# Kernel tuning notes

Measured on AMD Instinct MI355X. Metric: run time of the kernel, lower is better.

The kernel has to match this reference:

```python
import jax, jax.numpy as jnp
import numpy as np

N_EMBD = 1024
N_HEAD = 16
HEAD_DIM = N_EMBD // N_HEAD


def setup_inputs() -> dict:
    key = jax.random.key(0)
    ks = jax.random.split(key, 5)
    B, T, C = 2, 2048, N_EMBD
    scale = 0.02
    return {
        "x": jax.random.normal(ks[0], (B, T, C), dtype=jnp.float32),
        "w_attn": jax.random.normal(ks[1], (C, 3 * C), dtype=jnp.float32) * scale,
        "b_attn": jax.random.normal(ks[2], (3 * C,), dtype=jnp.float32) * scale,
        "w_proj": jax.random.normal(ks[3], (C, C), dtype=jnp.float32) * scale,
        "b_proj": jax.random.normal(ks[4], (C,), dtype=jnp.float32) * scale,
    }


def reference(x, w_attn, b_attn, w_proj, b_proj):
    B, T, C = x.shape
    H, D = N_HEAD, HEAD_DIM
    qkv = x @ w_attn + b_attn  # [B,T,3C]
    q, k, v = jnp.split(qkv, 3, axis=-1)
    # [B,T,C] -> [B,H,T,D]
    q = q.reshape(B, T, H, D).transpose(0, 2, 1, 3)
    k = k.reshape(B, T, H, D).transpose(0, 2, 1, 3)
    v = v.reshape(B, T, H, D).transpose(0, 2, 1, 3)
    scores = jnp.einsum("bhqd,bhkd->bhqk", q, k) / jnp.sqrt(jnp.float32(D))
    causal = jnp.tril(jnp.ones((T, T), dtype=bool))
    scores = jnp.where(causal, scores, jnp.finfo(scores.dtype).min)
    attn = jax.nn.softmax(scores, axis=-1)
    y = jnp.einsum("bhqk,bhkd->bhqd", attn, v)  # [B,H,T,D]
    y = y.transpose(0, 2, 1, 3).reshape(B, T, C)
    return y @ w_proj + b_proj
```

## Files before the change

kernel.cpp:

```cpp
#include <hip/hip_runtime.h>

typedef unsigned short u16;
typedef u16 u16x4 __attribute__((ext_vector_type(4)));
typedef u16 u16x8 __attribute__((ext_vector_type(8)));
typedef __bf16 bf16x8 __attribute__((ext_vector_type(8)));
typedef float floatx4 __attribute__((ext_vector_type(4)));

#define N_EMBD 1024
#define N_HEAD 16
#define HEAD_DIM 64
#define SEQ 2048
#define BATCH 2
#define M_ROWS (BATCH * SEQ)

typedef __attribute__((address_space(1))) const unsigned char ga_t;
typedef __attribute__((address_space(3))) unsigned char la_t;

#if __has_builtin(__builtin_amdgcn_exp2f)
#define EXP2(x) __builtin_amdgcn_exp2f(x)
#else
#define EXP2(x) exp2f(x)
#endif

__device__ __forceinline__ u16 cvt_bf16(float f) {
  return __builtin_bit_cast(u16, (__bf16)f);
}

__global__ __launch_bounds__(256) void prep(const float* __restrict__ x,
                                            u16* __restrict__ xb,
                                            const float* __restrict__ wa,
                                            const float* __restrict__ wp,
                                            u16* __restrict__ outa,
                                            u16* __restrict__ outp) {
  const int bid = blockIdx.x;
  if (bid < 2048) {
    const long i = ((long)bid * 256 + threadIdx.x) * 8;
    const float4 f0 = *(const float4*)&x[i];
    const float4 f1 = *(const float4*)&x[i + 4];
    u16x8 p;
    p[0] = cvt_bf16(f0.x); p[1] = cvt_bf16(f0.y);
    p[2] = cvt_bf16(f0.z); p[3] = cvt_bf16(f0.w);
    p[4] = cvt_bf16(f1.x); p[5] = cvt_bf16(f1.y);
    p[6] = cvt_bf16(f1.z); p[7] = cvt_bf16(f1.w);
    *(u16x8*)&xb[i] = p;
    return;
  }
  __shared__ u16 tile[32][33];
  const int t = bid - 2048;
  const int gx = t & 127;
  const int gy = t >> 7;
  const int R = N_EMBD;
  const float* in;
  u16* out;
  int C, bx;
  if (gx < 96) {
    in = wa; out = outa; C = 3 * N_EMBD; bx = gx * 32;
  } else {
    in = wp; out = outp; C = N_EMBD; bx = (gx - 96) * 32;
  }
  const int by = gy * 32;
  const int tx = threadIdx.x & 31;
  const int ty = threadIdx.x >> 5;
#pragma unroll
  for (int j = 0; j < 32; j += 8)
    tile[ty + j][tx] = cvt_bf16(in[(long)(by + ty + j) * C + bx + tx]);
  __syncthreads();
#pragma unroll
  for (int j = 0; j < 32; j += 8)
    out[(long)(bx + ty + j) * R + by + tx] = tile[tx][ty + j];
}

#define BK 32

template <int MODE>
__global__ __launch_bounds__(256) void gemm128(
    const u16* __restrict__ A, const u16* __restrict__ Bt,
    const float* __restrict__ bias, float* __restrict__ out,
    u16* __restrict__ qo, u16* __restrict__ ko, u16* __restrict__ vo, int N,
    int K) {
  __shared__ u16 As[128 * BK];
  __shared__ u16 Bs[128 * BK];
  const int tid = threadIdx.x;
  const int bm = blockIdx.y * 128;
  const int bn = blockIdx.x * 128;
  const int w = tid >> 6;
  const int l = tid & 63;
  const int wm = (w >> 1) * 64;
  const int wn = (w & 1) * 64;
  const int m16 = l & 15;
  const int quad = l >> 4;
  const int lrow = l >> 2;
  const int lcol = (l & 3) * 8;

  floatx4 acc[4][4];
#pragma unroll
  for (int i = 0; i < 4; ++i)
#pragma unroll
    for (int j = 0; j < 4; ++j) acc[i][j] = (floatx4){0.f, 0.f, 0.f, 0.f};

  for (int kt = 0; kt < K; kt += BK) {
#pragma unroll
    for (int p = 0; p < 2; ++p) {
      const int arow = p * 64 + w * 16;
      long gA;
      if (MODE == 0) {
        gA = (long)(bm + arow + lrow) * K + kt + lcol;
      } else {
        const int m = bm + arow + lrow;
        const int b = m >> 11, t = m & 2047;
        const int k0 = kt + lcol;
        const int head = k0 >> 6, dd = k0 & 63;
        gA = (((long)(b * N_HEAD + head)) * SEQ + t) * HEAD_DIM + dd;
      }
      __builtin_amdgcn_global_load_lds((ga_t*)(A + gA), (la_t*)&As[arow * BK],
                                       16, 0, 0);
      const long gB = (long)(bn + arow + lrow) * K + kt + lcol;
      __builtin_amdgcn_global_load_lds((ga_t*)(Bt + gB), (la_t*)&Bs[arow * BK],
                                       16, 0, 0);
    }
    __syncthreads();

    bf16x8 af[4], bfr[4];
#pragma unroll
    for (int i = 0; i < 4; ++i)
      af[i] = __builtin_bit_cast(
          bf16x8, *(const u16x8*)&As[(wm + i * 16 + m16) * BK + quad * 8]);
#pragma unroll
    for (int j = 0; j < 4; ++j)
      bfr[j] = __builtin_bit_cast(
          bf16x8, *(const u16x8*)&Bs[(wn + j * 16 + m16) * BK + quad * 8]);
#pragma unroll
    for (int i = 0; i < 4; ++i)
#pragma unroll
      for (int j = 0; j < 4; ++j)
        acc[i][j] = __builtin_amdgcn_mfma_f32_16x16x32_bf16(af[i], bfr[j],
                                                            acc[i][j], 0, 0, 0);
    __syncthreads();
  }

#pragma unroll
  for (int i = 0; i < 4; ++i) {
#pragma unroll
    for (int j = 0; j < 4; ++j) {
      const int col = bn + wn + j * 16 + m16;
      const float bv = bias[col];
      if (MODE == 1) {
#pragma unroll
        for (int r = 0; r < 4; ++r) {
          const int row = bm + wm + i * 16 + quad * 4 + r;
          out[(long)row * N_EMBD + col] = acc[i][j][r] + bv;
        }
      } else {
        const int which = col >> 10;
        const int cc = col & 1023;
        const int h = cc >> 6;
        const int dd = cc & 63;
        const int row0 = bm + wm + i * 16 + quad * 4;
        const int b = row0 >> 11;
        const int t0 = row0 & 2047;
        if (which == 2) {
          u16x4 pk;
#pragma unroll
          for (int r = 0; r < 4; ++r) pk[r] = cvt_bf16(acc[i][j][r] + bv);
          *(u16x4*)&vo[(((long)(b * N_HEAD + h)) * HEAD_DIM + dd) * SEQ + t0] =
              pk;
        } else {
          u16* dst = (which == 0) ? qo : ko;
#pragma unroll
          for (int r = 0; r < 4; ++r)
            dst[(((long)(b * N_HEAD + h)) * SEQ + t0 + r) * HEAD_DIM + dd] =
                cvt_bf16(acc[i][j][r] + bv);
        }
      }
    }
  }
}

#define BQ 64
#define BKV 64
#define LOG2E 1.44269504f
#define NQT (SEQ / BQ)

__device__ __forceinline__ void stage_kv(const u16* __restrict__ K,
                                         const u16* __restrict__ Vt, long bh,
                                         int kt, int tid, u16* kl, u16* vl) {
#pragma unroll
  for (int i = 0; i < 2; ++i) {
    const int p = tid + 256 * i;
    const int row = p >> 3;
    const int slot = (p & 7) ^ (row & 7);
    const int wb = (i * 256 + (tid & 192)) * 8;
    __builtin_amdgcn_global_load_lds(
        (ga_t*)&K[(bh * SEQ + kt + row) * HEAD_DIM + slot * 8], (la_t*)&kl[wb],
        16, 0, 0);
    __builtin_amdgcn_global_load_lds(
        (ga_t*)&Vt[(bh * HEAD_DIM + row) * SEQ + kt + slot * 8], (la_t*)&vl[wb],
        16, 0, 0);
  }
}

__global__ __launch_bounds__(256, 4) void flash_attn(
    u16* __restrict__ Qy, const u16* __restrict__ K,
    const u16* __restrict__ Vt) {
  const int id = blockIdx.x;
  const int iq = (NQT - 1) - (id >> 5);
  const int bh_ = ((id >> 3) & 3) * 8 + (id & 7);
  const long bh = bh_;
  const int tid = threadIdx.x;
  const int w = tid >> 6;
  const int l = tid & 63;
  const int m16 = l & 15;
  const int quad = l >> 4;

  __shared__ u16 Kl[2][BKV * 64];
  __shared__ u16 Vl[2][64 * BKV];
  __shared__ u16 Pl[4][16 * 64];

  const float SC = 0.125f * LOG2E;
  const int qb = iq * BQ;
  const int ntiles = iq + 1;
  const int qglob = qb + w * 16 + m16;
  const int sw = (m16 & 7) << 3;

  bf16x8 qf[2];
  {
    const u16* qrow = Qy + (bh * SEQ + qglob) * HEAD_DIM;
    qf[0] = __builtin_bit_cast(bf16x8, *(const u16x8*)&qrow[quad * 8]);
    qf[1] = __builtin_bit_cast(bf16x8, *(const u16x8*)&qrow[32 + quad * 8]);
  }

  floatx4 Oacc[4];
#pragma unroll
  for (int t = 0; t < 4; ++t) Oacc[t] = (floatx4){0.f, 0.f, 0.f, 0.f};
  float mrow = -1e30f, lrow = 0.f;

  stage_kv(K, Vt, bh, 0, tid, Kl[0], Vl[0]);
  __syncthreads();

  for (int it = 0; it < ntiles; ++it) {
    const int buf = it & 1;
    const int kt = it * BKV;
    if (it + 1 < ntiles)
      stage_kv(K, Vt, bh, kt + BKV, tid, Kl[buf ^ 1], Vl[buf ^ 1]);

    floatx4 s[4];
#pragma unroll
    for (int j = 0; j < 4; ++j) s[j] = (floatx4){0.f, 0.f, 0.f, 0.f};
#pragma unroll
    for (int j = 0; j < 4; ++j)
#pragma unroll
      for (int kk = 0; kk < 2; ++kk) {
        const bf16x8 kf = __builtin_bit_cast(
            bf16x8, *(const u16x8*)&Kl[buf][(j * 16 + m16) * 64 +
                                            ((kk * 32 + quad * 8) ^ sw)]);
        s[j] = __builtin_amdgcn_mfma_f32_16x16x32_bf16(kf, qf[kk], s[j], 0, 0,
                                                       0);
      }
    if (it == ntiles - 1) {
#pragma unroll
      for (int j = 0; j < 4; ++j) {
        const int key0 = kt + j * 16 + quad * 4;
#pragma unroll
        for (int r = 0; r < 4; ++r)
          if (key0 + r > qglob) s[j][r] = -1e30f;
      }
    }

    float t0 = fmaxf(fmaxf(s[0][0], s[0][1]), fmaxf(s[0][2], s[0][3]));
    float t1 = fmaxf(fmaxf(s[1][0], s[1][1]), fmaxf(s[1][2], s[1][3]));
    float t2 = fmaxf(fmaxf(s[2][0], s[2][1]), fmaxf(s[2][2], s[2][3]));
    float t3 = fmaxf(fmaxf(s[3][0], s[3][1]), fmaxf(s[3][2], s[3][3]));
    float tm = fmaxf(fmaxf(t0, t1), fmaxf(t2, t3));
    tm = fmaxf(tm, __shfl_xor(tm, 16, 64));
    tm = fmaxf(tm, __shfl_xor(tm, 32, 64));
    const float pm = tm * SC;
    if (!__all(pm <= mrow + 4.f)) {
      const float mn = fmaxf(mrow, pm);
      const float al = EXP2(mrow - mn);
      mrow = mn;
      lrow *= al;
#pragma unroll
      for (int t = 0; t < 4; ++t)
#pragma unroll
        for (int r = 0; r < 4; ++r) Oacc[t][r] *= al;
    }

    float ls = 0.f;
#pragma unroll
    for (int j = 0; j < 4; ++j) {
      u16x4 pk;
#pragma unroll
      for (int r = 0; r < 4; ++r) {
        const float p = EXP2(__builtin_fmaf(s[j][r], SC, -mrow));
        ls += p;
        pk[r] = cvt_bf16(p);
      }
      *(u16x4*)&Pl[w][m16 * 64 + ((j * 16 + quad * 4) ^ sw)] = pk;
    }
    ls += __shfl_xor(ls, 16, 64);
    ls += __shfl_xor(ls, 32, 64);
    lrow += ls;

    bf16x8 pf[2];
    pf[0] = __builtin_bit_cast(
        bf16x8, *(const u16x8*)&Pl[w][m16 * 64 + ((quad * 8) ^ sw)]);
    pf[1] = __builtin_bit_cast(
        bf16x8, *(const u16x8*)&Pl[w][m16 * 64 + ((32 + quad * 8) ^ sw)]);
#pragma unroll
    for (int t = 0; t < 4; ++t)
#pragma unroll
      for (int kk = 0; kk < 2; ++kk) {
        const bf16x8 vf = __builtin_bit_cast(
            bf16x8, *(const u16x8*)&Vl[buf][(t * 16 + m16) * 64 +
                                            ((kk * 32 + quad * 8) ^ sw)]);
        Oacc[t] = __builtin_amdgcn_mfma_f32_16x16x32_bf16(vf, pf[kk], Oacc[t],
                                                          0, 0, 0);
      }
    __syncthreads();
  }

  const float invl = 1.f / lrow;
#pragma unroll
  for (int t = 0; t < 4; ++t) {
    u16x4 pk;
#pragma unroll
    for (int r = 0; r < 4; ++r) pk[r] = cvt_bf16(Oacc[t][r] * invl);
    *(u16x4*)&Qy[(bh * SEQ + qglob) * HEAD_DIM + t * 16 + quad * 4] = pk;
  }
}

extern "C" void kernel_launch(void* const* d_in, const int* in_sizes, int n_in,
                              void* d_out, int out_size, void* d_ws,
                              size_t ws_size, hipStream_t stream) {
  const float* x = (const float*)d_in[0];
  const float* w_attn = (const float*)d_in[1];
  const float* b_attn = (const float*)d_in[2];
  const float* w_proj = (const float*)d_in[3];
  const float* b_proj = (const float*)d_in[4];
  float* out = (float*)d_out;

  char* ws = (char*)d_ws;
  const size_t SZ = (size_t)BATCH * N_HEAD * SEQ * HEAD_DIM * sizeof(u16);
  u16* q = (u16*)(ws);
  u16* k = (u16*)(ws + SZ);
  u16* vT = (u16*)(ws + 2 * SZ);
  u16* wT_a = (u16*)(ws + 3 * SZ);
  u16* wT_p = (u16*)(ws + 3 * SZ + (size_t)3 * N_EMBD * N_EMBD * sizeof(u16));
  u16* xb = (u16*)(ws + 3 * SZ + (size_t)4 * N_EMBD * N_EMBD * sizeof(u16));

  prep<<<2048 + 4096, 256, 0, stream>>>(x, xb, w_attn, w_proj, wT_a, wT_p);

  gemm128<0><<<dim3(3 * N_EMBD / 128, M_ROWS / 128), 256, 0, stream>>>(
      xb, wT_a, b_attn, nullptr, q, k, vT, 3 * N_EMBD, N_EMBD);

  flash_attn<<<NQT * 32, 256, 0, stream>>>(q, k, vT);

  gemm128<1><<<dim3(N_EMBD / 128, M_ROWS / 128), 256, 0, stream>>>(
      q, wT_p, b_proj, out, nullptr, nullptr, nullptr, N_EMBD, N_EMBD);
}
```

Measured before the change: 192.3 us.

## Double-buffer GEMM LDS tiles, swizzle k-chunks, and remap workgroup order

The GEMM kernel now uses two LDS buffers per operand, so the global-to-LDS load of the next K tile is issued before the MFMAs run on the current tile, with one barrier per iteration. The k-chunk each lane loads and reads is XOR-swizzled by row to reduce LDS bank conflicts on the 16-byte fragment reads. Workgroup IDs are also remapped with a stride-8 permutation to change how tiles are spread across XCDs for cache locality. This doubles LDS use per block, which may lower occupancy, and the remap assumes the workgroup count is divisible by 8.

```diff
diff --git a/kernel.cpp b/kernel.cpp
--- a/kernel.cpp
+++ b/kernel.cpp
@@ -73,24 +73,60 @@
 #define BK 32
 
 template <int MODE>
+__device__ __forceinline__ void stage128(const u16* __restrict__ A,
+                                         const u16* __restrict__ Bt, int bm,
+                                         int bn, int kt, int K, int tid,
+                                         u16* as, u16* bs) {
+  const int w = tid >> 6;
+  const int l = tid & 63;
+  const int lrow = l >> 2;
+#pragma unroll
+  for (int p = 0; p < 2; ++p) {
+    const int arow = p * 64 + w * 16;
+    const int row = arow + lrow;
+    const int sl = (l & 3) ^ ((row >> 1) & 3);
+    long gA;
+    if (MODE == 0) {
+      gA = (long)(bm + row) * K + kt + sl * 8;
+    } else {
+      const int m = bm + row;
+      const int b = m >> 11, t = m & 2047;
+      const int k0 = kt + sl * 8;
+      const int head = k0 >> 6, dd = k0 & 63;
+      gA = (((long)(b * N_HEAD + head)) * SEQ + t) * HEAD_DIM + dd;
+    }
+    __builtin_amdgcn_global_load_lds((ga_t*)(A + gA), (la_t*)&as[arow * BK],
+                                     16, 0, 0);
+    const long gB = (long)(bn + row) * K + kt + sl * 8;
+    __builtin_amdgcn_global_load_lds((ga_t*)(Bt + gB), (la_t*)&bs[arow * BK],
+                                     16, 0, 0);
+  }
+}
+
+template <int MODE>
 __global__ __launch_bounds__(256) void gemm128(
     const u16* __restrict__ A, const u16* __restrict__ Bt,
     const float* __restrict__ bias, float* __restrict__ out,
     u16* __restrict__ qo, u16* __restrict__ ko, u16* __restrict__ vo, int N,
     int K) {
-  __shared__ u16 As[128 * BK];
-  __shared__ u16 Bs[128 * BK];
+  __shared__ u16 As[2][128 * BK];
+  __shared__ u16 Bs[2][128 * BK];
   const int tid = threadIdx.x;
-  const int bm = blockIdx.y * 128;
-  const int bn = blockIdx.x * 128;
+
+  const int nx = gridDim.x;
+  const int nwg = nx * gridDim.y;
+  int lin = blockIdx.y * nx + blockIdx.x;
+  lin = (lin & 7) * (nwg >> 3) + (lin >> 3);
+  const int bm = (lin / nx) * 128;
+  const int bn = (lin % nx) * 128;
+
   const int w = tid >> 6;
   const int l = tid & 63;
   const int wm = (w >> 1) * 64;
   const int wn = (w & 1) * 64;
   const int m16 = l & 15;
   const int quad = l >> 4;
-  const int lrow = l >> 2;
-  const int lcol = (l & 3) * 8;
+  const int ksw = (quad ^ ((m16 >> 1) & 3)) * 8;
 
   floatx4 acc[4][4];
 #pragma unroll
@@ -98,37 +134,25 @@
 #pragma unroll
     for (int j = 0; j < 4; ++j) acc[i][j] = (floatx4){0.f, 0.f, 0.f, 0.f};
 
-  for (int kt = 0; kt < K; kt += BK) {
-#pragma unroll
-    for (int p = 0; p < 2; ++p) {
-      const int arow = p * 64 + w * 16;
-      long gA;
-      if (MODE == 0) {
-        gA = (long)(bm + arow + lrow) * K + kt + lcol;
-      } else {
-        const int m = bm + arow + lrow;
-        const int b = m >> 11, t = m & 2047;
-        const int k0 = kt + lcol;
-        const int head = k0 >> 6, dd = k0 & 63;
-        gA = (((long)(b * N_HEAD + head)) * SEQ + t) * HEAD_DIM + dd;
-      }
-      __builtin_amdgcn_global_load_lds((ga_t*)(A + gA), (la_t*)&As[arow * BK],
-                                       16, 0, 0);
-      const long gB = (long)(bn + arow + lrow) * K + kt + lcol;
-      __builtin_amdgcn_global_load_lds((ga_t*)(Bt + gB), (la_t*)&Bs[arow * BK],
-                                       16, 0, 0);
-    }
-    __syncthreads();
+  const int nk = K / BK;
+  stage128<MODE>(A, Bt, bm, bn, 0, K, tid, As[0], Bs[0]);
+  __syncthreads();
+
+  int cur = 0;
+  for (int t = 0; t < nk; ++t) {
+    if (t + 1 < nk)
+      stage128<MODE>(A, Bt, bm, bn, (t + 1) * BK, K, tid, As[cur ^ 1],
+                     Bs[cur ^ 1]);
 
     bf16x8 af[4], bfr[4];
 #pragma unroll
     for (int i = 0; i < 4; ++i)
       af[i] = __builtin_bit_cast(
-          bf16x8, *(const u16x8*)&As[(wm + i * 16 + m16) * BK + quad * 8]);
+          bf16x8, *(const u16x8*)&As[cur][(wm + i * 16 + m16) * BK + ksw]);
 #pragma unroll
     for (int j = 0; j < 4; ++j)
       bfr[j] = __builtin_bit_cast(
-          bf16x8, *(const u16x8*)&Bs[(wn + j * 16 + m16) * BK + quad * 8]);
+          bf16x8, *(const u16x8*)&Bs[cur][(wn + j * 16 + m16) * BK + ksw]);
 #pragma unroll
     for (int i = 0; i < 4; ++i)
 #pragma unroll
@@ -136,6 +160,7 @@
         acc[i][j] = __builtin_amdgcn_mfma_f32_16x16x32_bf16(af[i], bfr[j],
                                                             acc[i][j], 0, 0, 0);
     __syncthreads();
+    cur ^= 1;
   }
 
 #pragma unroll
```

After: 182.1 us. -5.3%, faster.
